# Kernel tuning notes

Hardware: AMD Instinct MI355X
Metric: run time of the kernel (lower is better)

## Reference

```python
import jax, jax.numpy as jnp
import numpy as np

N_NODES = 400_000
N_EDGES = 1_600_000
N_GRAPHS = 16_384
MOL_DIM = 32
META_DIM = 16
HIDDEN = 64
NUM_SPECIES = 50
FUSION = 2 * HIDDEN + HIDDEN + 16  # mean+max pool (128) + meta (64) + species emb (16) = 208


def setup_inputs() -> dict:
    key = jax.random.key(0)
    ks = jax.random.split(key, 20)
    s = lambda *sh: sh
    inp = {
        "x": jax.random.normal(ks[0], (N_NODES, MOL_DIM), jnp.float32),
        "metadata": jax.random.normal(ks[1], (N_GRAPHS, META_DIM), jnp.float32),
        "edge_index": jax.random.randint(ks[2], (2, N_EDGES), 0, N_NODES),
        "batch": jnp.sort(jax.random.randint(ks[3], (N_NODES,), 0, N_GRAPHS)),
        "species_id": jax.random.randint(ks[4], (N_GRAPHS,), 0, NUM_SPECIES),
        # GCN layer params
        "W1": jax.random.normal(ks[5], (MOL_DIM, HIDDEN), jnp.float32) / np.sqrt(MOL_DIM),
        "b1": jnp.zeros((HIDDEN,), jnp.float32),
        "W2": jax.random.normal(ks[6], (HIDDEN, HIDDEN), jnp.float32) / np.sqrt(HIDDEN),
        "b2": jnp.zeros((HIDDEN,), jnp.float32),
        "W3": jax.random.normal(ks[7], (HIDDEN, HIDDEN), jnp.float32) / np.sqrt(HIDDEN),
        "b3": jnp.zeros((HIDDEN,), jnp.float32),
        # meta encoder
        "Wm": jax.random.normal(ks[8], (META_DIM, HIDDEN), jnp.float32) / np.sqrt(META_DIM),
        "bm": jnp.zeros((HIDDEN,), jnp.float32),
        "species_emb": jax.random.normal(ks[9], (NUM_SPECIES, 16), jnp.float32),
        # predictor
        "Wp1": jax.random.normal(ks[10], (FUSION, 64), jnp.float32) / np.sqrt(FUSION),
        "bp1": jnp.zeros((64,), jnp.float32),
        "Wp2": jax.random.normal(ks[11], (64, 1), jnp.float32) / 8.0,
        "bp2": jnp.zeros((1,), jnp.float32),
    }
    return inp


def _gcn_conv(x, W, b, row, col, dinv):
    # x' = D^{-1/2}(A+I)D^{-1/2} x W + b  (PyG GCNConv with self-loops)
    h = x @ W                                   # [N, out]
    norm = dinv[row] * dinv[col]                # [E]
    msg = norm[:, None] * h[col]                # [E, out]
    agg = jax.ops.segment_sum(msg, row, num_segments=x.shape[0])
    agg = agg + (dinv * dinv)[:, None] * h      # self-loop term
    return agg + b


def reference(x, metadata, edge_index, batch, species_id,
              W1, b1, W2, b2, W3, b3, Wm, bm, species_emb, Wp1, bp1, Wp2, bp2):
    row, col = edge_index[0], edge_index[1]
    deg = jax.ops.segment_sum(jnp.ones_like(row, jnp.float32), row,
                              num_segments=N_NODES) + 1.0  # +1 self loop
    dinv = jax.lax.rsqrt(deg)

    h = jax.nn.relu(_gcn_conv(x, W1, b1, row, col, dinv))
    h = jax.nn.relu(_gcn_conv(h, W2, b2, row, col, dinv))
    h = jax.nn.relu(_gcn_conv(h, W3, b3, row, col, dinv))

    counts = jax.ops.segment_sum(jnp.ones((N_NODES,), jnp.float32), batch,
                                 num_segments=N_GRAPHS)
    mean = jax.ops.segment_sum(h, batch, num_segments=N_GRAPHS) / \
           jnp.maximum(counts, 1.0)[:, None]
    mx = jax.ops.segment_max(h, batch, num_segments=N_GRAPHS)
    mx = jnp.where(counts[:, None] > 0, mx, 0.0)
    graph_embed = jnp.concatenate([mean, mx], axis=1)     # [G, 128]

    meta = jax.nn.relu(metadata @ Wm + bm)                 # [G, 64]
    meta_embed = jnp.concatenate([meta, species_emb[species_id]], axis=1)

    fused = jnp.concatenate([graph_embed, meta_embed], axis=1)  # [G, 208]
    out = jax.nn.relu(fused @ Wp1 + bp1) @ Wp2 + bp2       # dropout off (eval)
    return out
```

## Files before the change

### kernel.cpp

```cpp
#include <hip/hip_runtime.h>
#include <hip/hip_bf16.h>

#define N_NODES 400000
#define N_EDGES 1600000
#define N_GRAPHS 16384
#define CHUNK 50
#define NCHUNK (N_NODES / CHUNK)

#define BSHIFT 11
#define BKT_N (1 << BSHIFT)
#define NBKT ((N_NODES + BKT_N - 1) >> BSHIFT)
#define BIN_CHUNK 4096

typedef __attribute__((ext_vector_type(8))) short bf16x8;
typedef __attribute__((ext_vector_type(4))) float f32x4;
typedef unsigned short bfu;

__device__ __forceinline__ float rlane(float x, int k) {
    return __int_as_float(__builtin_amdgcn_readlane(__float_as_int(x), k));
}
__device__ __forceinline__ int rlanei(int x, int k) {
    return __builtin_amdgcn_readlane(x, k);
}

__device__ __forceinline__ short f2bf(float x) {
    unsigned u = __float_as_uint(x);
    unsigned r = (u + 0x7fffu + ((u >> 16) & 1u)) >> 16;
    return (short)r;
}
__device__ __forceinline__ float bf2f(short b) {
    return __uint_as_float(((unsigned)(unsigned short)b) << 16);
}
__device__ __forceinline__ float bfu2f(bfu b) {
    return __uint_as_float(((unsigned)b) << 16);
}

__global__ __launch_bounds__(256) void k_bcnt(const int* __restrict__ rows,
                                              int* __restrict__ bkt, int E) {
    __shared__ int l[NBKT];
    const int t = threadIdx.x;
    for (int i = t; i < NBKT; i += 256) l[i] = 0;
    __syncthreads();
    const int e0 = blockIdx.x * BIN_CHUNK;
#pragma unroll
    for (int k = 0; k < 16; ++k) {
        int e = e0 + k * 256 + t;
        if (e < E) atomicAdd(&l[rows[e] >> BSHIFT], 1);
    }
    __syncthreads();
    for (int i = t; i < NBKT; i += 256)
        if (l[i]) atomicAdd(&bkt[i], l[i]);
}

__global__ void k_bscan(const int* __restrict__ bkt, int* __restrict__ bbase,
                        int* __restrict__ bcur) {
    __shared__ int s[256];
    const int t = threadIdx.x;
    int v = (t < NBKT) ? bkt[t] : 0;
    s[t] = v; __syncthreads();
    for (int off = 1; off < 256; off <<= 1) {
        int x = (t >= off) ? s[t - off] : 0;
        __syncthreads();
        s[t] += x;
        __syncthreads();
    }
    int excl = s[t] - v;
    if (t < NBKT) { bbase[t] = excl; bcur[t] = excl; }
    if (t == NBKT) bbase[NBKT] = excl;
}

__global__ __launch_bounds__(256) void k_bin(const int* __restrict__ rows,
                                             const int* __restrict__ cols,
                                             int* __restrict__ bcur,
                                             int2* __restrict__ tmp, int E) {
    __shared__ int lcnt[NBKT];
    __shared__ int lbase[NBKT];
    const int t = threadIdx.x;
    const int e0 = blockIdx.x * BIN_CHUNK;
    for (int i = t; i < NBKT; i += 256) lcnt[i] = 0;
    __syncthreads();
    int r[16];
#pragma unroll
    for (int k = 0; k < 16; ++k) {
        int e = e0 + k * 256 + t;
        r[k] = (e < E) ? rows[e] : -1;
        if (r[k] >= 0) atomicAdd(&lcnt[r[k] >> BSHIFT], 1);
    }
    __syncthreads();
    for (int i = t; i < NBKT; i += 256) lbase[i] = atomicAdd(&bcur[i], lcnt[i]);
    __syncthreads();
    for (int i = t; i < NBKT; i += 256) lcnt[i] = 0;
    __syncthreads();
#pragma unroll
    for (int k = 0; k < 16; ++k) {
        int e = e0 + k * 256 + t;
        if (r[k] >= 0) {
            int b = r[k] >> BSHIFT;
            int p = lbase[b] + atomicAdd(&lcnt[b], 1);
            tmp[p] = make_int2(r[k], cols[e]);
        }
    }
}

__global__ __launch_bounds__(256) void k_csr(const int2* __restrict__ tmp,
                                             const int* __restrict__ bbase,
                                             int* __restrict__ row_ptr,
                                             float* __restrict__ dinv,
                                             int* __restrict__ colsOut,
                                             int N, int E) {
    __shared__ int lcnt[BKT_N];
    __shared__ int lofs[BKT_N];
    __shared__ int tsum[256];
    const int t = threadIdx.x;
    const int b = blockIdx.x;
    const int r0 = b << BSHIFT;
    const int S = bbase[b];
    const int T = bbase[b + 1];
    for (int i = t; i < BKT_N; i += 256) lcnt[i] = 0;
    __syncthreads();
    for (int e = S + t; e < T; e += 256) atomicAdd(&lcnt[tmp[e].x - r0], 1);
    __syncthreads();
    const int base8 = t * 8;
    int vals[8];
    int run = 0;
#pragma unroll
    for (int k = 0; k < 8; ++k) { vals[k] = run; run += lcnt[base8 + k]; }
    tsum[t] = run;
    __syncthreads();
    for (int off = 1; off < 256; off <<= 1) {
        int x = (t >= off) ? tsum[t - off] : 0;
        __syncthreads();
        tsum[t] += x;
        __syncthreads();
    }
    const int texcl = tsum[t] - run;
#pragma unroll
    for (int k = 0; k < 8; ++k) lofs[base8 + k] = texcl + vals[k];
    __syncthreads();
    for (int i = t; i < BKT_N; i += 256) {
        int node = r0 + i;
        if (node < N) {
            row_ptr[node] = S + lofs[i];
            dinv[node] = rsqrtf((float)lcnt[i] + 1.0f);
        }
    }
    if (b == 0 && t == 0) row_ptr[N] = E;
    __syncthreads();
    for (int e = S + t; e < T; e += 256) {
        int2 rc = tmp[e];
        int pos = S + atomicAdd(&lofs[rc.x - r0], 1);
        colsOut[pos] = rc.y;
    }
}

__global__ void k_gb(const int* __restrict__ batch, int* __restrict__ gstart,
                     int N, int G) {
    int i = blockIdx.x * blockDim.x + threadIdx.x;
    if (i <= N) {
        int b = (i < N) ? batch[i] : G;
        int prev = (i == 0) ? -1 : batch[i - 1];
        for (int g = prev + 1; g <= b; ++g) gstart[g] = i;
    }
}

template <int IN_D, bool PRESCALE, bool ABF16>
__global__ __launch_bounds__(256, 4) void k_gemm_mfma(
        const void* __restrict__ in_, const float* __restrict__ W,
        const float* __restrict__ dinv, bfu* __restrict__ out, int nTiles) {
    constexpr int KT = IN_D / 32;
    const int lane = threadIdx.x & 63;
    const int m = lane & 15;
    const int q = lane >> 4;

    bf16x8 Bhi[4][KT], Blo[4][KT];
#pragma unroll
    for (int nt = 0; nt < 4; ++nt) {
#pragma unroll
        for (int kt = 0; kt < KT; ++kt) {
#pragma unroll
            for (int j = 0; j < 8; ++j) {
                int k = kt * 32 + q * 8 + j;
                float w = W[k * 64 + nt * 16 + m];
                short hi = f2bf(w);
                Bhi[nt][kt][j] = hi;
                Blo[nt][kt][j] = f2bf(w - bf2f(hi));
            }
        }
    }

    const int wv = (blockIdx.x * 256 + threadIdx.x) >> 6;
    const int nwv = (gridDim.x * 256) >> 6;

    for (int tile = wv; tile < nTiles; tile += nwv) {
        const int node0 = tile * 16;
        f32x4 C[4];
#pragma unroll
        for (int nt = 0; nt < 4; ++nt) C[nt] = (f32x4){0.f, 0.f, 0.f, 0.f};

        if (ABF16) {
            const bfu* rowb = (const bfu*)in_ + (size_t)(node0 + m) * IN_D + q * 8;
            bf16x8 A[KT];
#pragma unroll
            for (int kt = 0; kt < KT; ++kt) A[kt] = *(const bf16x8*)(rowb + kt * 32);
#pragma unroll
            for (int nt = 0; nt < 4; ++nt) {
#pragma unroll
                for (int kt = 0; kt < KT; ++kt) {
                    C[nt] = __builtin_amdgcn_mfma_f32_16x16x32_bf16(A[kt], Bhi[nt][kt], C[nt], 0, 0, 0);
                    C[nt] = __builtin_amdgcn_mfma_f32_16x16x32_bf16(A[kt], Blo[nt][kt], C[nt], 0, 0, 0);
                }
            }
        } else {
            const float dv = PRESCALE ? dinv[node0 + m] : 1.0f;
            const float* rowp = (const float*)in_ + (size_t)(node0 + m) * IN_D + q * 8;
            bf16x8 Ahi[KT], Alo[KT];
#pragma unroll
            for (int kt = 0; kt < KT; ++kt) {
                f32x4 a0 = *(const f32x4*)(rowp + kt * 32);
                f32x4 a1 = *(const f32x4*)(rowp + kt * 32 + 4);
#pragma unroll
                for (int j = 0; j < 4; ++j) {
                    float xx = PRESCALE ? dv * a0[j] : a0[j];
                    short hi = f2bf(xx);
                    Ahi[kt][j] = hi;
                    Alo[kt][j] = f2bf(xx - bf2f(hi));
                }
#pragma unroll
                for (int j = 0; j < 4; ++j) {
                    float xx = PRESCALE ? dv * a1[j] : a1[j];
                    short hi = f2bf(xx);
                    Ahi[kt][4 + j] = hi;
                    Alo[kt][4 + j] = f2bf(xx - bf2f(hi));
                }
            }
#pragma unroll
            for (int nt = 0; nt < 4; ++nt) {
#pragma unroll
                for (int kt = 0; kt < KT; ++kt) {
                    C[nt] = __builtin_amdgcn_mfma_f32_16x16x32_bf16(Ahi[kt], Bhi[nt][kt], C[nt], 0, 0, 0);
                    C[nt] = __builtin_amdgcn_mfma_f32_16x16x32_bf16(Ahi[kt], Blo[nt][kt], C[nt], 0, 0, 0);
                    C[nt] = __builtin_amdgcn_mfma_f32_16x16x32_bf16(Alo[kt], Bhi[nt][kt], C[nt], 0, 0, 0);
                }
            }
        }

        bfu* op = out + (size_t)node0 * 64;
#pragma unroll
        for (int nt = 0; nt < 4; ++nt) {
#pragma unroll
            for (int r = 0; r < 4; ++r) {
                op[(size_t)(q * 4 + r) * 64 + nt * 16 + m] = (bfu)f2bf(C[nt][r]);
            }
        }
    }
}

template <int POOL>
__global__ __launch_bounds__(256, 8) void k_agg_seg(
        const bfu* __restrict__ M, const float* __restrict__ bias,
        const int* __restrict__ row_ptr, const int* __restrict__ cols,
        const float* __restrict__ dinv, const int* __restrict__ batch,
        bfu* __restrict__ out, float* __restrict__ psum,
        float* __restrict__ pmax) {
    const int lane = threadIdx.x & 63;
    int wid = (blockIdx.x * blockDim.x + threadIdx.x) >> 6;
    wid = __builtin_amdgcn_readfirstlane(wid);
    const int nw = (gridDim.x * blockDim.x) >> 6;
    const float b = bias[lane];
    const bfu* Ml = M + lane;

    for (int c = wid; c < NCHUNK; c += nw) {
        const int i0 = c * CHUNK;
        const int rpn = row_ptr[i0 + min(lane, CHUNK - 1) + 1];
        const int S = row_ptr[i0];
        const int ne = rlanei(rpn, CHUNK - 1) - S;
        const float dvv = dinv[i0 + min(lane, CHUNK - 1)];
        const int bvv = POOL ? batch[i0 + min(lane, CHUNK - 1)] : 0;

        int node = 0;
        int bnd = rlanei(rpn, 0) - S;
        float acc = 0.0f;
        float selfA = bfu2f(Ml[(size_t)i0 * 64]);
        float selfB = bfu2f(Ml[(size_t)(i0 + 1) * 64]);
        float selfC = bfu2f(Ml[(size_t)(i0 + 2) * 64]);
        int gcur = POOL ? rlanei(bvv, 0) : 0;
        float rsum = 0.0f, rmax = 0.0f;

        auto flush = [&]() {
            if (POOL) {
                atomicAdd(&psum[(size_t)gcur * 64 + lane], rsum);
                atomicMax((int*)&pmax[(size_t)gcur * 64 + lane], __float_as_int(rmax));
            }
        };
        auto finalize = [&]() {
            const float d = rlane(dvv, node);
            const float h = fmaxf(fmaf(d, selfA + acc, b), 0.0f);
            if (POOL) {
                const int g = rlanei(bvv, node);
                if (g != gcur) { flush(); gcur = g; rsum = 0.0f; rmax = 0.0f; }
                rsum += h;
                rmax = fmaxf(rmax, h);
            } else {
                out[(size_t)(i0 + node) * 64 + lane] = (bfu)f2bf(d * h);
            }
            acc = 0.0f;
            selfA = selfB;
            selfB = selfC;
            if (node + 3 < CHUNK) selfC = bfu2f(Ml[(size_t)(i0 + node + 3) * 64]);
            ++node;
            if (node < CHUNK) bnd = rlanei(rpn, node) - S;
        };

        if (ne > 0) {
            int bidx = 0;
            int a0 = S + lane, a1 = S + 64 + lane;
            int colv0 = (a0 < S + ne) ? cols[a0] : 0;
            int colv1 = (a1 < S + ne) ? cols[a1] : 0;
            unsigned ubuf[16];
#pragma unroll
            for (int k = 0; k < 16; ++k) {
                int e = min(k, ne - 1);
                int cc = rlanei(colv0, e);
                ubuf[k] = Ml[(size_t)cc * 64];
            }

            int j = 0;
            while (j + 16 <= ne) {
#pragma unroll
                for (int k = 0; k < 16; ++k) {
                    const int jj = j + k;
                    if ((jj & 63) == 0 && jj != 0) {
                        colv0 = colv1;
                        ++bidx;
                        int ad = S + (bidx + 1) * 64 + lane;
                        colv1 = (ad < S + ne) ? cols[ad] : 0;
                    }
                    while (jj == bnd) finalize();
                    acc += __uint_as_float(ubuf[k] << 16);
                    int ec = min(jj + 16, ne - 1);
                    int src = ((ec >> 6) == bidx) ? colv0 : colv1;
                    int cc = rlanei(src, ec & 63);
                    ubuf[k] = Ml[(size_t)cc * 64];
                }
                j += 16;
            }
            for (; j < ne; ++j) {
                while (j == bnd) finalize();
                acc += __uint_as_float(ubuf[j & 15] << 16);
            }
        }
        while (node < CHUNK) finalize();
        flush();
    }
}

__global__ __launch_bounds__(256) void k_asm(
        const float* __restrict__ psum, const float* __restrict__ pmax,
        const int* __restrict__ gstart, const float* __restrict__ metadata,
        const int* __restrict__ species, const float* __restrict__ emb,
        const float* __restrict__ Wm, const float* __restrict__ bm,
        float* __restrict__ fused, int G) {
    const int lane = threadIdx.x & 63;
    int wv = (blockIdx.x * blockDim.x + threadIdx.x) >> 6;
    const int nw = (gridDim.x * blockDim.x) >> 6;
    const float bmr = bm[lane];
    float wmr[16];
#pragma unroll
    for (int k = 0; k < 16; ++k) wmr[k] = Wm[k * 64 + lane];
    for (int g = wv; g < G; g += nw) {
        float gc = (float)(gstart[g + 1] - gstart[g]);
        float mean = psum[(size_t)g * 64 + lane] / fmaxf(gc, 1.0f);
        float mx = pmax[(size_t)g * 64 + lane];
        float md = lane < 16 ? metadata[(size_t)g * 16 + lane] : 0.0f;
        float mval = bmr;
#pragma unroll
        for (int k = 0; k < 16; ++k) mval = fmaf(rlane(md, k), wmr[k], mval);
        mval = fmaxf(mval, 0.0f);
        const int sid = species[g];
        float* fr = fused + (size_t)g * 224;
        fr[lane] = mean;
        fr[64 + lane] = mx;
        fr[128 + lane] = mval;
        if (lane < 16) fr[192 + lane] = emb[(size_t)sid * 16 + lane];
        else if (lane < 32) fr[192 + lane] = 0.0f;
    }
}

__global__ __launch_bounds__(256, 2) void k_pred_mfma(
        const float* __restrict__ fused, const float* __restrict__ Wp1,
        const float* __restrict__ bp1, const float* __restrict__ Wp2,
        const float* __restrict__ bp2, float* __restrict__ out, int G) {
    __shared__ __align__(16) short Whi[64 * 232];
    __shared__ __align__(16) short Wlo[64 * 232];
    const int t = threadIdx.x;
    for (int idx = t; idx < 64 * 232; idx += 256) {
        int n = idx / 232;
        int k = idx % 232;
        float w = (k < 208) ? Wp1[(size_t)k * 64 + n] : 0.0f;
        short hi = f2bf(w);
        Whi[n * 232 + k] = hi;
        Wlo[n * 232 + k] = f2bf(w - bf2f(hi));
    }
    __syncthreads();

    const int lane = t & 63;
    const int wave = t >> 6;
    const int m = lane & 15;
    const int q = lane >> 4;
    const int g0 = (blockIdx.x * 4 + wave) * 16;
    if (g0 >= G) return;

    const float* rowp = fused + (size_t)(g0 + m) * 224 + q * 8;

    f32x4 C[4];
#pragma unroll
    for (int nt = 0; nt < 4; ++nt) C[nt] = (f32x4){0.f, 0.f, 0.f, 0.f};

#pragma unroll
    for (int kt = 0; kt < 7; ++kt) {
        f32x4 a0 = *(const f32x4*)(rowp + kt * 32);
        f32x4 a1 = *(const f32x4*)(rowp + kt * 32 + 4);
        bf16x8 Ahi, Alo;
#pragma unroll
        for (int j = 0; j < 4; ++j) {
            short hi = f2bf(a0[j]);
            Ahi[j] = hi;
            Alo[j] = f2bf(a0[j] - bf2f(hi));
        }
#pragma unroll
        for (int j = 0; j < 4; ++j) {
            short hi = f2bf(a1[j]);
            Ahi[4 + j] = hi;
            Alo[4 + j] = f2bf(a1[j] - bf2f(hi));
        }
#pragma unroll
        for (int nt = 0; nt < 4; ++nt) {
            const int boff = (nt * 16 + m) * 232 + kt * 32 + q * 8;
            bf16x8 Bh = *(const bf16x8*)&Whi[boff];
            bf16x8 Bl = *(const bf16x8*)&Wlo[boff];
            C[nt] = __builtin_amdgcn_mfma_f32_16x16x32_bf16(Ahi, Bh, C[nt], 0, 0, 0);
            C[nt] = __builtin_amdgcn_mfma_f32_16x16x32_bf16(Ahi, Bl, C[nt], 0, 0, 0);
            C[nt] = __builtin_amdgcn_mfma_f32_16x16x32_bf16(Alo, Bh, C[nt], 0, 0, 0);
        }
    }

    float wp2r[4], bp1r[4];
#pragma unroll
    for (int nt = 0; nt < 4; ++nt) {
        wp2r[nt] = Wp2[nt * 16 + m];
        bp1r[nt] = bp1[nt * 16 + m];
    }
    const float bp2v = bp2[0];
    float s[4];
#pragma unroll
    for (int r = 0; r < 4; ++r) {
        float acc = 0.0f;
#pragma unroll
        for (int nt = 0; nt < 4; ++nt)
            acc += fmaxf(C[nt][r] + bp1r[nt], 0.0f) * wp2r[nt];
        s[r] = acc;
    }
#pragma unroll
    for (int off = 1; off < 16; off <<= 1) {
#pragma unroll
        for (int r = 0; r < 4; ++r) s[r] += __shfl_xor(s[r], off);
    }
    if (m == 0) {
#pragma unroll
        for (int r = 0; r < 4; ++r) out[g0 + q * 4 + r] = s[r] + bp2v;
    }
}

extern "C" void kernel_launch(void* const* d_in, const int* in_sizes, int n_in,
                              void* d_out, int out_size, void* d_ws, size_t ws_size,
                              hipStream_t stream) {
    const int N = N_NODES, E = N_EDGES, G = N_GRAPHS;

    const float* x        = (const float*)d_in[0];
    const float* metadata = (const float*)d_in[1];
    const int*   ei       = (const int*)d_in[2];
    const int*   batch    = (const int*)d_in[3];
    const int*   species  = (const int*)d_in[4];
    const float* W1 = (const float*)d_in[5];
    const float* b1 = (const float*)d_in[6];
    const float* W2 = (const float*)d_in[7];
    const float* b2 = (const float*)d_in[8];
    const float* W3 = (const float*)d_in[9];
    const float* b3 = (const float*)d_in[10];
    const float* Wm = (const float*)d_in[11];
    const float* bm = (const float*)d_in[12];
    const float* emb = (const float*)d_in[13];
    const float* Wp1 = (const float*)d_in[14];
    const float* bp1 = (const float*)d_in[15];
    const float* Wp2 = (const float*)d_in[16];
    const float* bp2 = (const float*)d_in[17];
    float* out = (float*)d_out;

    char* ws = (char*)d_ws;
    size_t off = 0;
    auto alloc = [&](size_t bytes) -> void* {
        void* p = ws + off;
        off = (off + bytes + 255) & ~(size_t)255;
        return p;
    };
    int*   row_ptr = (int*)alloc((size_t)(N + 1) * 4);
    float* dinv    = (float*)alloc((size_t)N * 4);
    int*   gstart  = (int*)alloc((size_t)(G + 1) * 4);
    int*   bkt     = (int*)alloc((size_t)NBKT * 4);
    int*   bbase   = (int*)alloc((size_t)(NBKT + 1) * 4);
    int*   bcur    = (int*)alloc((size_t)NBKT * 4);
    int*   colsS   = (int*)alloc((size_t)E * 4);
    float* psum    = (float*)alloc((size_t)G * 64 * 4);
    float* pmax    = (float*)alloc((size_t)G * 64 * 4);
    bfu*   Mb      = (bfu*)alloc((size_t)N * 64 * 2);
    bfu*   hb      = (bfu*)alloc((size_t)N * 64 * 2);
    float* fused   = (float*)alloc((size_t)G * 224 * 4);

    int2* tmp = (int2*)Mb;

    const int nbBin = (E + BIN_CHUNK - 1) / BIN_CHUNK;

    hipMemsetAsync(bkt, 0, (size_t)NBKT * 4, stream);
    hipMemsetAsync(psum, 0, (size_t)G * 64 * 4, stream);
    hipMemsetAsync(pmax, 0, (size_t)G * 64 * 4, stream);

    k_bcnt<<<nbBin, 256, 0, stream>>>(ei, bkt, E);
    k_bscan<<<1, 256, 0, stream>>>(bkt, bbase, bcur);
    k_bin<<<nbBin, 256, 0, stream>>>(ei, ei + E, bcur, tmp, E);
    k_csr<<<NBKT, 256, 0, stream>>>(tmp, bbase, row_ptr, dinv, colsS, N, E);
    k_gb<<<(N + 256) / 256 + 1, 256, 0, stream>>>(batch, gstart, N, G);

    const int nTiles = N / 16;
    const int nbAgg = NCHUNK / 4;
    k_gemm_mfma<32, true, false><<<1563, 256, 0, stream>>>(x, W1, dinv, Mb, nTiles);
    k_agg_seg<0><<<nbAgg, 256, 0, stream>>>(Mb, b1, row_ptr, colsS, dinv, batch,
                                            hb, psum, pmax);
    k_gemm_mfma<64, false, true><<<1563, 256, 0, stream>>>(hb, W2, dinv, Mb, nTiles);
    k_agg_seg<0><<<nbAgg, 256, 0, stream>>>(Mb, b2, row_ptr, colsS, dinv, batch,
                                            hb, psum, pmax);
    k_gemm_mfma<64, false, true><<<1563, 256, 0, stream>>>(hb, W3, dinv, Mb, nTiles);
    k_agg_seg<1><<<nbAgg, 256, 0, stream>>>(Mb, b3, row_ptr, colsS, dinv, batch,
                                            hb, psum, pmax);

    k_asm<<<512, 256, 0, stream>>>(psum, pmax, gstart, metadata, species, emb, Wm, bm,
                                   fused, G);
    k_pred_mfma<<<(G / 16 + 3) / 4, 256, 0, stream>>>(fused, Wp1, bp1, Wp2, bp2, out, G);
}
```

Baseline: 478.8 us.

## Fuse CSR-build preprocessing kernels, shrink buckets, merge memsets into one

Merges the bucket-count and graph-boundary kernels into one launch, drops the single-block scan kernel by having each binning block redo the bucket prefix scan and each CSR block reduce its own base offset, and merges three memsets into a single contiguous memset. The bucket size shrinks from 2048 to 512 nodes, giving about four times as many buckets with more, smaller CSR blocks. This removes several launches and serial gaps in preprocessing. The cost is redundant scan work in every binning block, per-block reductions in the CSR kernel, and more global atomics on the larger bucket array.

```diff
diff --git a/kernel.cpp b/kernel.cpp
--- a/kernel.cpp
+++ b/kernel.cpp
@@ -7,10 +7,11 @@
 #define CHUNK 50
 #define NCHUNK (N_NODES / CHUNK)
 
-#define BSHIFT 11
+#define BSHIFT 9
 #define BKT_N (1 << BSHIFT)
 #define NBKT ((N_NODES + BKT_N - 1) >> BSHIFT)
 #define BIN_CHUNK 4096
+#define NBBIN ((N_EDGES + BIN_CHUNK - 1) / BIN_CHUNK)
 
 typedef __attribute__((ext_vector_type(8))) short bf16x8;
 typedef __attribute__((ext_vector_type(4))) float f32x4;
@@ -35,50 +36,48 @@
     return __uint_as_float(((unsigned)b) << 16);
 }
 
-__global__ __launch_bounds__(256) void k_bcnt(const int* __restrict__ rows,
-                                              int* __restrict__ bkt, int E) {
+__global__ __launch_bounds__(256) void k_bcnt_gb(const int* __restrict__ rows,
+                                                 int* __restrict__ bkt,
+                                                 const int* __restrict__ batch,
+                                                 int* __restrict__ gstart,
+                                                 int N, int G, int E) {
     __shared__ int l[NBKT];
     const int t = threadIdx.x;
-    for (int i = t; i < NBKT; i += 256) l[i] = 0;
-    __syncthreads();
-    const int e0 = blockIdx.x * BIN_CHUNK;
-#pragma unroll
-    for (int k = 0; k < 16; ++k) {
-        int e = e0 + k * 256 + t;
-        if (e < E) atomicAdd(&l[rows[e] >> BSHIFT], 1);
-    }
-    __syncthreads();
-    for (int i = t; i < NBKT; i += 256)
-        if (l[i]) atomicAdd(&bkt[i], l[i]);
-}
-
-__global__ void k_bscan(const int* __restrict__ bkt, int* __restrict__ bbase,
-                        int* __restrict__ bcur) {
-    __shared__ int s[256];
-    const int t = threadIdx.x;
-    int v = (t < NBKT) ? bkt[t] : 0;
-    s[t] = v; __syncthreads();
-    for (int off = 1; off < 256; off <<= 1) {
-        int x = (t >= off) ? s[t - off] : 0;
-        __syncthreads();
-        s[t] += x;
-        __syncthreads();
-    }
-    int excl = s[t] - v;
-    if (t < NBKT) { bbase[t] = excl; bcur[t] = excl; }
-    if (t == NBKT) bbase[NBKT] = excl;
+    const int b = blockIdx.x;
+    int i = b * 256 + t;
+    if (i <= N) {
+        int bb = (i < N) ? batch[i] : G;
+        int prev = (i == 0) ? -1 : batch[i - 1];
+        for (int g = prev + 1; g <= bb; ++g) gstart[g] = i;
+    }
+    if (b < NBBIN) {
+        for (int k = t; k < NBKT; k += 256) l[k] = 0;
+        __syncthreads();
+        const int e0 = b * BIN_CHUNK;
+#pragma unroll
+        for (int k = 0; k < 16; ++k) {
+            int e = e0 + k * 256 + t;
+            if (e < E) atomicAdd(&l[rows[e] >> BSHIFT], 1);
+        }
+        __syncthreads();
+        for (int k = t; k < NBKT; k += 256)
+            if (l[k]) atomicAdd(&bkt[k], l[k]);
+    }
 }
 
 __global__ __launch_bounds__(256) void k_bin(const int* __restrict__ rows,
                                              const int* __restrict__ cols,
-                                             int* __restrict__ bcur,
+                                             const int* __restrict__ bkt,
+                                             int* __restrict__ bcur0,
                                              int2* __restrict__ tmp, int E) {
     __shared__ int lcnt[NBKT];
+    __shared__ int gbase[NBKT];
     __shared__ int lbase[NBKT];
+    __shared__ int tsum[256];
     const int t = threadIdx.x;
+    for (int i = t; i < NBKT; i += 256) lcnt[i] = 0;
+    __syncthreads();
     const int e0 = blockIdx.x * BIN_CHUNK;
-    for (int i = t; i < NBKT; i += 256) lcnt[i] = 0;
-    __syncthreads();
     int r[16];
 #pragma unroll
     for (int k = 0; k < 16; ++k) {
@@ -86,24 +85,50 @@
         r[k] = (e < E) ? rows[e] : -1;
         if (r[k] >= 0) atomicAdd(&lcnt[r[k] >> BSHIFT], 1);
     }
-    __syncthreads();
-    for (int i = t; i < NBKT; i += 256) lbase[i] = atomicAdd(&bcur[i], lcnt[i]);
+    const int base4 = t * 4;
+    int v[4];
+    int run = 0;
+#pragma unroll
+    for (int k = 0; k < 4; ++k) {
+        int idx = base4 + k;
+        int x = (idx < NBKT) ? bkt[idx] : 0;
+        v[k] = run;
+        run += x;
+    }
+    tsum[t] = run;
+    __syncthreads();
+    for (int off = 1; off < 256; off <<= 1) {
+        int x = (t >= off) ? tsum[t - off] : 0;
+        __syncthreads();
+        tsum[t] += x;
+        __syncthreads();
+    }
+    const int texcl = tsum[t] - run;
+#pragma unroll
+    for (int k = 0; k < 4; ++k) {
+        int idx = base4 + k;
+        if (idx < NBKT) gbase[idx] = texcl + v[k];
+    }
+    __syncthreads();
+    for (int i = t; i < NBKT; i += 256) {
+        int c = lcnt[i];
+        lbase[i] = c ? (gbase[i] + atomicAdd(&bcur0[i], c)) : 0;
+    }
     __syncthreads();
     for (int i = t; i < NBKT; i += 256) lcnt[i] = 0;
     __syncthreads();
 #pragma unroll
     for (int k = 0; k < 16; ++k) {
-        int e = e0 + k * 256 + t;
         if (r[k] >= 0) {
             int b = r[k] >> BSHIFT;
             int p = lbase[b] + atomicAdd(&lcnt[b], 1);
-            tmp[p] = make_int2(r[k], cols[e]);
+            tmp[p] = make_int2(r[k], cols[e0 + k * 256 + t]);
         }
     }
 }
 
 __global__ __launch_bounds__(256) void k_csr(const int2* __restrict__ tmp,
-                                             const int* __restrict__ bbase,
+                                             const int* __restrict__ bkt,
                                              int* __restrict__ row_ptr,
                                              float* __restrict__ dinv,
                                              int* __restrict__ colsOut,
@@ -114,17 +139,26 @@
     const int t = threadIdx.x;
     const int b = blockIdx.x;
     const int r0 = b << BSHIFT;
-    const int S = bbase[b];
-    const int T = bbase[b + 1];
+    int part = 0;
+    for (int i = t; i < b; i += 256) part += bkt[i];
+    tsum[t] = part;
+    __syncthreads();
+    for (int off = 128; off > 0; off >>= 1) {
+        if (t < off) tsum[t] += tsum[t + off];
+        __syncthreads();
+    }
+    const int S = tsum[0];
+    const int T = S + bkt[b];
+    __syncthreads();
     for (int i = t; i < BKT_N; i += 256) lcnt[i] = 0;
     __syncthreads();
     for (int e = S + t; e < T; e += 256) atomicAdd(&lcnt[tmp[e].x - r0], 1);
     __syncthreads();
-    const int base8 = t * 8;
-    int vals[8];
+    const int base2 = t * 2;
+    int vals[2];
     int run = 0;
 #pragma unroll
-    for (int k = 0; k < 8; ++k) { vals[k] = run; run += lcnt[base8 + k]; }
+    for (int k = 0; k < 2; ++k) { vals[k] = run; run += lcnt[base2 + k]; }
     tsum[t] = run;
     __syncthreads();
     for (int off = 1; off < 256; off <<= 1) {
@@ -135,7 +169,7 @@
     }
     const int texcl = tsum[t] - run;
 #pragma unroll
-    for (int k = 0; k < 8; ++k) lofs[base8 + k] = texcl + vals[k];
+    for (int k = 0; k < 2; ++k) lofs[base2 + k] = texcl + vals[k];
     __syncthreads();
     for (int i = t; i < BKT_N; i += 256) {
         int node = r0 + i;
@@ -150,16 +184,6 @@
         int2 rc = tmp[e];
         int pos = S + atomicAdd(&lofs[rc.x - r0], 1);
         colsOut[pos] = rc.y;
-    }
-}
-
-__global__ void k_gb(const int* __restrict__ batch, int* __restrict__ gstart,
-                     int N, int G) {
-    int i = blockIdx.x * blockDim.x + threadIdx.x;
-    if (i <= N) {
-        int b = (i < N) ? batch[i] : G;
-        int prev = (i == 0) ? -1 : batch[i - 1];
-        for (int g = prev + 1; g <= b; ++g) gstart[g] = i;
     }
 }
 
@@ -506,29 +530,25 @@
     int*   row_ptr = (int*)alloc((size_t)(N + 1) * 4);
     float* dinv    = (float*)alloc((size_t)N * 4);
     int*   gstart  = (int*)alloc((size_t)(G + 1) * 4);
+    size_t z0 = off;
     int*   bkt     = (int*)alloc((size_t)NBKT * 4);
-    int*   bbase   = (int*)alloc((size_t)(NBKT + 1) * 4);
     int*   bcur    = (int*)alloc((size_t)NBKT * 4);
-    int*   colsS   = (int*)alloc((size_t)E * 4);
     float* psum    = (float*)alloc((size_t)G * 64 * 4);
     float* pmax    = (float*)alloc((size_t)G * 64 * 4);
+    size_t zlen = off - z0;
+    int*   colsS   = (int*)alloc((size_t)E * 4);
     bfu*   Mb      = (bfu*)alloc((size_t)N * 64 * 2);
     bfu*   hb      = (bfu*)alloc((size_t)N * 64 * 2);
     float* fused   = (float*)alloc((size_t)G * 224 * 4);
 
     int2* tmp = (int2*)Mb;
 
-    const int nbBin = (E + BIN_CHUNK - 1) / BIN_CHUNK;
-
-    hipMemsetAsync(bkt, 0, (size_t)NBKT * 4, stream);
-    hipMemsetAsync(psum, 0, (size_t)G * 64 * 4, stream);
-    hipMemsetAsync(pmax, 0, (size_t)G * 64 * 4, stream);
-
-    k_bcnt<<<nbBin, 256, 0, stream>>>(ei, bkt, E);
-    k_bscan<<<1, 256, 0, stream>>>(bkt, bbase, bcur);
-    k_bin<<<nbBin, 256, 0, stream>>>(ei, ei + E, bcur, tmp, E);
-    k_csr<<<NBKT, 256, 0, stream>>>(tmp, bbase, row_ptr, dinv, colsS, N, E);
-    k_gb<<<(N + 256) / 256 + 1, 256, 0, stream>>>(batch, gstart, N, G);
+    hipMemsetAsync(ws + z0, 0, zlen, stream);
+
+    const int nbGb = (N + 256) / 256 + 1;
+    k_bcnt_gb<<<nbGb, 256, 0, stream>>>(ei, bkt, batch, gstart, N, G, E);
+    k_bin<<<NBBIN, 256, 0, stream>>>(ei, ei + E, bkt, bcur, tmp, E);
+    k_csr<<<NBKT, 256, 0, stream>>>(tmp, bkt, row_ptr, dinv, colsS, N, E);
 
     const int nTiles = N / 16;
     const int nbAgg = NCHUNK / 4;
```

Measured after the change: 477.9 us. About the same (-0.2%).
